# Performance work log

Hardware: AMD Instinct MI355X
Metric: run time of the kernel (lower is better)

Reference implementation:

```python
import jax, jax.numpy as jnp
import numpy as np

B, T, F, H = 128, 1024, 64, 256


def _lstm_cell(x, h, c, W_ih, W_hh, b):
    # x: [B,F], h,c: [B,H]; gate order i,f,g,o (PyTorch convention)
    gates = x @ W_ih.T + h @ W_hh.T + b  # [B,4H]
    i, f, g, o = jnp.split(gates, 4, axis=-1)
    i, f, o = jax.nn.sigmoid(i), jax.nn.sigmoid(f), jax.nn.sigmoid(o)
    g = jnp.tanh(g)
    c = f * c + i * g
    h = o * jnp.tanh(c)
    return h, c


def setup_inputs() -> dict:
    key = jax.random.key(0)
    ks = jax.random.split(key, 10)
    s = 1.0 / np.sqrt(H)
    inp = {
        "ts_batch": jax.random.normal(ks[0], (B, T, F), jnp.float32),
        "W_ih_enc": jax.random.uniform(ks[1], (4 * H, F), jnp.float32, -s, s),
        "W_hh_enc": jax.random.uniform(ks[2], (4 * H, H), jnp.float32, -s, s),
        "b_enc": jax.random.uniform(ks[3], (4 * H,), jnp.float32, -s, s),
        "W_ih_dec": jax.random.uniform(ks[4], (4 * H, F), jnp.float32, -s, s),
        "W_hh_dec": jax.random.uniform(ks[5], (4 * H, H), jnp.float32, -s, s),
        "b_dec": jax.random.uniform(ks[6], (4 * H,), jnp.float32, -s, s),
        "W_out": jax.random.uniform(ks[7], (F, H), jnp.float32, -s, s),
        "b_out": jax.random.uniform(ks[8], (F,), jnp.float32, -s, s),
    }
    return inp


def reference(ts_batch, W_ih_enc, W_hh_enc, b_enc, W_ih_dec, W_hh_dec, b_dec, W_out, b_out):
    batch = ts_batch.shape[0]
    hidden = W_hh_enc.shape[1]
    xs = jnp.swapaxes(ts_batch, 0, 1)  # [T,B,F]

    # ---- encoder: full-sequence LSTM, keep only final (h,c) ----
    def enc_step(carry, x):
        h, c = carry
        h, c = _lstm_cell(x, h, c, W_ih_enc, W_hh_enc, b_enc)
        return (h, c), None

    h0 = jnp.zeros((batch, hidden), ts_batch.dtype)
    (h, c), _ = jax.lax.scan(enc_step, (h0, h0), xs)

    # ---- decoder: iterate timesteps in reverse; emit projection of the
    # hidden state BEFORE consuming the input at that step (training branch) ----
    def dec_step(carry, x):
        h, c = carry
        out = h @ W_out.T + b_out  # [B,F]
        h, c = _lstm_cell(x, h, c, W_ih_dec, W_hh_dec, b_dec)
        return (h, c), out

    _, outs_rev = jax.lax.scan(dec_step, (h, c), xs[::-1])  # [T,B,F], reversed time
    return jnp.swapaxes(outs_rev[::-1], 0, 1)  # [B,T,F]
```

## Files before the change

### kernel.cpp

```cpp
#include <hip/hip_runtime.h>
#include <hip/hip_bf16.h>


#define Bb 128
#define Tt 1024
#define Ff 64
#define Hh 256

typedef _Float16 h16;
typedef __attribute__((ext_vector_type(8))) _Float16 h16x8;
typedef __attribute__((ext_vector_type(4))) float f32x4;

#define WENC_OFF 0
#define WDEC_OFF 327680
#define WOUT_OFF 655360
#define HBUF_OFF 671744
#define FLAGS_BYTE_OFF 1474560

__device__ __forceinline__ float fast_sigmoid(float x) {
  float e = __expf(-fabsf(x));
  float s = __builtin_amdgcn_rcpf(1.f + e);
  return x >= 0.f ? s : 1.f - s;
}
__device__ __forceinline__ float fast_tanh(float x) {
  float e = __expf(-2.f * fabsf(x));
  float r = (1.f - e) * __builtin_amdgcn_rcpf(1.f + e);
  return x >= 0.f ? r : -r;
}

__global__ void lstm_prep(const float* __restrict__ Wih_e, const float* __restrict__ Whh_e,
                          const float* __restrict__ Wih_d, const float* __restrict__ Whh_d,
                          const float* __restrict__ Wout, h16* __restrict__ ws16,
                          unsigned int* __restrict__ flags) {
  int e = blockIdx.x * 256 + threadIdx.x;
  if (e < 16) flags[e] = 0u;
  if (e < 655360) {
    int r = e;
    const float* Wih = Wih_e; const float* Whh = Whh_e;
    int off = WENC_OFF;
    if (r >= 327680) { r -= 327680; Wih = Wih_d; Whh = Whh_d; off = WDEC_OFF; }
    int j    = r & 7;
    int lane = (r >> 3) & 63;
    int kt   = (r >> 9) % 10;
    int tmp  = (r >> 9) / 10;
    int nt   = tmp & 7;
    int w    = (tmp >> 3) & 3;
    int q    = tmp >> 5;
    int g = nt >> 1, ct = nt & 1;
    int col = q * 128 + w * 32 + ct * 16 + (lane & 15);
    int row = g * 256 + col;
    int k = kt * 32 + (lane >> 4) * 8 + j;
    float v = (k < 64) ? Wih[row * 64 + k] : Whh[row * 256 + (k - 64)];
    ws16[off + r] = (h16)v;
  } else if (e < 655360 + 16384) {
    int r = e - 655360;
    int j    = r & 7;
    int lane = (r >> 3) & 63;
    int kt   = (r >> 9) & 7;
    int wt   = (r >> 12) & 1;
    int q    = (r >> 13) & 1;
    int f = q * 32 + wt * 16 + (lane & 15);
    int k = kt * 32 + (lane >> 4) * 8 + j;
    ws16[WOUT_OFF + r] = (h16)Wout[f * 256 + k];
  }
}

__global__ __launch_bounds__(256, 1) void lstm_main(
    const float* __restrict__ ts,
    const float* __restrict__ b_enc, const float* __restrict__ b_dec,
    const float* __restrict__ b_out,
    const h16* __restrict__ wsW, h16* __restrict__ hbuf,
    unsigned int* flags, float* __restrict__ out) {
  const int tid = threadIdx.x;
  const int wg = blockIdx.x;
  const int grp = wg & 7, q = wg >> 3;
  const int w = tid >> 6, lane = tid & 63;
  const int n16 = lane & 15, quad = lane >> 4;
  const int b0 = grp * 16;
  const int partner = wg ^ 8;

  __shared__ h16 xh[2][16][328];
  __shared__ h16x8 woutLds[1024];

  h16x8 wf[8][10];
  {
    const h16x8* wsrc = (const h16x8*)(wsW + WENC_OFF);
#pragma unroll
    for (int nt = 0; nt < 8; ++nt)
#pragma unroll
      for (int kt = 0; kt < 10; ++kt)
        wf[nt][kt] = wsrc[(((q * 4 + w) * 8 + nt) * 10 + kt) * 64 + lane];
  }
  float bias8[8];
#pragma unroll
  for (int nt = 0; nt < 8; ++nt) {
    int g = nt >> 1, ct = nt & 1;
    bias8[nt] = b_enc[g * 256 + q * 128 + w * 32 + ct * 16 + n16];
  }
  const float bo = b_out[q * 32 + w * 16 + n16];

  float c8[8];
#pragma unroll
  for (int i = 0; i < 8; ++i) c8[i] = 0.f;

  for (int i = tid; i < 16 * 264; i += 256) {
    int m = i / 264;
    xh[0][m][64 + (i - m * 264)] = (h16)0.f;
  }
  const int m_x = tid >> 4, ks_x = (tid & 15) * 4;
  {
    const f32x4 xv0 = *(const f32x4*)(ts + ((size_t)(b0 + m_x) * Tt + 0) * Ff + ks_x);
#pragma unroll
    for (int u = 0; u < 4; ++u) xh[0][m_x][ks_x + u] = (h16)xv0[u];
  }
  __syncthreads();

  for (int t = 0; t < 2048; ++t) {
    const int nb = t & 1, nxt = nb ^ 1;
    const bool dec = (t >= 1024);

    if (t > 0) {
      while (__hip_atomic_load(&flags[partner], __ATOMIC_ACQUIRE,
                               __HIP_MEMORY_SCOPE_AGENT) < (unsigned int)t)
        __builtin_amdgcn_s_sleep(1);
    }

    if (t == 1024) {
      const h16x8* wsrc2 = (const h16x8*)(wsW + WDEC_OFF);
#pragma unroll
      for (int nt = 0; nt < 8; ++nt)
#pragma unroll
        for (int kt = 0; kt < 10; ++kt)
          wf[nt][kt] = wsrc2[(((q * 4 + w) * 8 + nt) * 10 + kt) * 64 + lane];
#pragma unroll
      for (int nt = 0; nt < 8; ++nt) {
        int g = nt >> 1, ct = nt & 1;
        bias8[nt] = b_dec[g * 256 + q * 128 + w * 32 + ct * 16 + n16];
      }
      const h16x8* wo = (const h16x8*)(wsW + WOUT_OFF) + q * 1024;
      for (int i = tid; i < 1024; i += 256) woutLds[i] = wo[i];
      __syncthreads();
    }

    h16x8 a[10];
    const h16* xrow = &xh[nb][n16][0];
#pragma unroll
    for (int kt = 0; kt < 2; ++kt)
      a[kt] = *(const h16x8*)(xrow + kt * 32 + quad * 8);
    if (q == 0) {
#pragma unroll
      for (int i = 0; i < 4; ++i)
        a[2 + i] = *(const h16x8*)(xrow + (2 + i) * 32 + quad * 8);
    } else {
#pragma unroll
      for (int i = 0; i < 4; ++i)
        a[6 + i] = *(const h16x8*)(xrow + (6 + i) * 32 + quad * 8);
    }
    if (t > 0) {
      const h16x8* ps = (const h16x8*)(hbuf + ((size_t)partner * 2 + ((t + 1) & 1)) * 2048);
      if (q == 0) {
#pragma unroll
        for (int i = 0; i < 4; ++i) a[6 + i] = ps[n16 * 16 + i * 4 + quad];
      } else {
#pragma unroll
        for (int i = 0; i < 4; ++i) a[2 + i] = ps[n16 * 16 + i * 4 + quad];
      }
    } else {
      h16x8 z;
#pragma unroll
      for (int i = 0; i < 8; ++i) z[i] = (h16)0.f;
      if (q == 0) { a[6] = z; a[7] = z; a[8] = z; a[9] = z; }
      else        { a[2] = z; a[3] = z; a[4] = z; a[5] = z; }
    }

    f32x4 xv;
#pragma unroll
    for (int u = 0; u < 4; ++u) xv[u] = 0.f;
    if (t + 1 < 2048) {
      int xi = (t + 1 < 1024) ? (t + 1) : (2047 - (t + 1));
      xv = *(const f32x4*)(ts + ((size_t)(b0 + m_x) * Tt + xi) * Ff + ks_x);
    }

    f32x4 acc[8];
#pragma unroll
    for (int nt = 0; nt < 8; ++nt) {
      f32x4 v; v[0] = bias8[nt]; v[1] = bias8[nt]; v[2] = bias8[nt]; v[3] = bias8[nt];
      acc[nt] = v;
    }
#pragma unroll
    for (int kt = 0; kt < 10; ++kt)
#pragma unroll
      for (int nt = 0; nt < 8; ++nt)
        acc[nt] = __builtin_amdgcn_mfma_f32_16x16x32_f16(a[kt], wf[nt][kt], acc[nt], 0, 0, 0);

    h16 hv[8];
#pragma unroll
    for (int ct = 0; ct < 2; ++ct)
#pragma unroll
      for (int r = 0; r < 4; ++r) {
        float i_ = fast_sigmoid(acc[0 + ct][r]);
        float f_ = fast_sigmoid(acc[2 + ct][r]);
        float g_ = fast_tanh(acc[4 + ct][r]);
        float o_ = fast_sigmoid(acc[6 + ct][r]);
        float cv = f_ * c8[ct * 4 + r] + i_ * g_;
        c8[ct * 4 + r] = cv;
        hv[ct * 4 + r] = (h16)(o_ * fast_tanh(cv));
      }

    if (dec && w < 2) {
      f32x4 ao; ao[0] = bo; ao[1] = bo; ao[2] = bo; ao[3] = bo;
#pragma unroll
      for (int kt = 0; kt < 8; ++kt)
        ao = __builtin_amdgcn_mfma_f32_16x16x32_f16(a[2 + kt], woutLds[(w * 8 + kt) * 64 + lane], ao, 0, 0, 0);
      int tpos = 2047 - t;
      int f = q * 32 + w * 16 + n16;
#pragma unroll
      for (int r = 0; r < 4; ++r) {
        int m = quad * 4 + r;
        out[((size_t)(b0 + m) * Tt + tpos) * Ff + f] = ao[r];
      }
    }

    {
      h16* hb = hbuf + ((size_t)wg * 2 + (t & 1)) * 2048;
#pragma unroll
      for (int ct = 0; ct < 2; ++ct)
#pragma unroll
        for (int r = 0; r < 4; ++r) {
          int m = quad * 4 + r;
          int colLocal = w * 32 + ct * 16 + n16;
          xh[nxt][m][64 + q * 128 + colLocal] = hv[ct * 4 + r];
          hb[m * 128 + colLocal] = hv[ct * 4 + r];
        }
      if (t + 1 < 2048) {
#pragma unroll
        for (int u = 0; u < 4; ++u) xh[nxt][m_x][ks_x + u] = (h16)xv[u];
      }
    }

    __threadfence();
    __syncthreads();
    if (t < 2047 && tid == 0)
      __hip_atomic_store(&flags[wg], (unsigned int)(t + 1), __ATOMIC_RELEASE,
                         __HIP_MEMORY_SCOPE_AGENT);
  }
}

extern "C" void kernel_launch(void* const* d_in, const int* in_sizes, int n_in,
                              void* d_out, int out_size, void* d_ws, size_t ws_size,
                              hipStream_t stream) {
  const float* ts  = (const float*)d_in[0];
  const float* Wie = (const float*)d_in[1];
  const float* Whe = (const float*)d_in[2];
  const float* be  = (const float*)d_in[3];
  const float* Wid = (const float*)d_in[4];
  const float* Whd = (const float*)d_in[5];
  const float* bd  = (const float*)d_in[6];
  const float* Wo  = (const float*)d_in[7];
  const float* bo  = (const float*)d_in[8];

  h16* ws16 = (h16*)d_ws;
  unsigned int* flags = (unsigned int*)((char*)d_ws + FLAGS_BYTE_OFF);
  float* out = (float*)d_out;

  lstm_prep<<<2624, 256, 0, stream>>>(Wie, Whe, Wid, Whd, Wo, ws16, flags);
  lstm_main<<<16, 256, 0, stream>>>(ts, be, bd, bo, ws16, ws16 + HBUF_OFF, flags, out);
}
```

Baseline: 10.60 ms.

## Overlap local MFMA with partner wait and use per-wave relaxed flag counters

Each workgroup now runs the MFMAs for its own x and h slice before spinning on the partner's flag. The partner's half of h is then loaded with relaxed atomic loads and its MFMAs are finished afterwards. The wait on the partner moves later in the step and the partner-independent work overlaps it. Publishing changes from a threadfence plus single release store to coalesced 64-bit relaxed atomic stores staged through LDS, followed by s_waitcnt and a per-wave fetch_add on padded flag slots. The decoder output projection moves after the publish, off the critical path. The risk is memory-ordering correctness, because relaxed atomics and an empty asm barrier replace the acquire/release semantics.

```diff
diff --git a/kernel.cpp b/kernel.cpp
--- a/kernel.cpp
+++ b/kernel.cpp
@@ -10,6 +10,7 @@
 typedef _Float16 h16;
 typedef __attribute__((ext_vector_type(8))) _Float16 h16x8;
 typedef __attribute__((ext_vector_type(4))) float f32x4;
+typedef unsigned long long u64;
 
 #define WENC_OFF 0
 #define WDEC_OFF 327680
@@ -27,13 +28,18 @@
   float r = (1.f - e) * __builtin_amdgcn_rcpf(1.f + e);
   return x >= 0.f ? r : -r;
 }
+__device__ __forceinline__ h16x8 pack16(u64 lo, u64 hi) {
+  union { u64 u[2]; h16x8 v; } x;
+  x.u[0] = lo; x.u[1] = hi;
+  return x.v;
+}
 
 __global__ void lstm_prep(const float* __restrict__ Wih_e, const float* __restrict__ Whh_e,
                           const float* __restrict__ Wih_d, const float* __restrict__ Whh_d,
                           const float* __restrict__ Wout, h16* __restrict__ ws16,
                           unsigned int* __restrict__ flags) {
   int e = blockIdx.x * 256 + threadIdx.x;
-  if (e < 16) flags[e] = 0u;
+  if (e < 256) flags[e] = 0u;
   if (e < 655360) {
     int r = e;
     const float* Wih = Wih_e; const float* Whh = Whh_e;
@@ -65,6 +71,17 @@
   }
 }
 
+#define MFMA_KT(kt) do {                                                         \
+    acc[0] = __builtin_amdgcn_mfma_f32_16x16x32_f16(a[kt], wf[0][kt], acc[0], 0, 0, 0); \
+    acc[1] = __builtin_amdgcn_mfma_f32_16x16x32_f16(a[kt], wf[1][kt], acc[1], 0, 0, 0); \
+    acc[2] = __builtin_amdgcn_mfma_f32_16x16x32_f16(a[kt], wf[2][kt], acc[2], 0, 0, 0); \
+    acc[3] = __builtin_amdgcn_mfma_f32_16x16x32_f16(a[kt], wf[3][kt], acc[3], 0, 0, 0); \
+    acc[4] = __builtin_amdgcn_mfma_f32_16x16x32_f16(a[kt], wf[4][kt], acc[4], 0, 0, 0); \
+    acc[5] = __builtin_amdgcn_mfma_f32_16x16x32_f16(a[kt], wf[5][kt], acc[5], 0, 0, 0); \
+    acc[6] = __builtin_amdgcn_mfma_f32_16x16x32_f16(a[kt], wf[6][kt], acc[6], 0, 0, 0); \
+    acc[7] = __builtin_amdgcn_mfma_f32_16x16x32_f16(a[kt], wf[7][kt], acc[7], 0, 0, 0); \
+  } while (0)
+
 __global__ __launch_bounds__(256, 1) void lstm_main(
     const float* __restrict__ ts,
     const float* __restrict__ b_enc, const float* __restrict__ b_dec,
@@ -79,7 +96,7 @@
   const int b0 = grp * 16;
   const int partner = wg ^ 8;
 
-  __shared__ h16 xh[2][16][328];
+  __shared__ __align__(16) h16 xh[2][16][328];
   __shared__ h16x8 woutLds[1024];
 
   h16x8 wf[8][10];
@@ -119,12 +136,6 @@
     const int nb = t & 1, nxt = nb ^ 1;
     const bool dec = (t >= 1024);
 
-    if (t > 0) {
-      while (__hip_atomic_load(&flags[partner], __ATOMIC_ACQUIRE,
-                               __HIP_MEMORY_SCOPE_AGENT) < (unsigned int)t)
-        __builtin_amdgcn_s_sleep(1);
-    }
-
     if (t == 1024) {
       const h16x8* wsrc2 = (const h16x8*)(wsW + WDEC_OFF);
 #pragma unroll
@@ -144,34 +155,29 @@
 
     h16x8 a[10];
     const h16* xrow = &xh[nb][n16][0];
-#pragma unroll
-    for (int kt = 0; kt < 2; ++kt)
-      a[kt] = *(const h16x8*)(xrow + kt * 32 + quad * 8);
+    a[0] = *(const h16x8*)(xrow + 0 * 32 + quad * 8);
+    a[1] = *(const h16x8*)(xrow + 1 * 32 + quad * 8);
     if (q == 0) {
-#pragma unroll
-      for (int i = 0; i < 4; ++i)
-        a[2 + i] = *(const h16x8*)(xrow + (2 + i) * 32 + quad * 8);
+      a[2] = *(const h16x8*)(xrow + 2 * 32 + quad * 8);
+      a[3] = *(const h16x8*)(xrow + 3 * 32 + quad * 8);
+      a[4] = *(const h16x8*)(xrow + 4 * 32 + quad * 8);
+      a[5] = *(const h16x8*)(xrow + 5 * 32 + quad * 8);
     } else {
-#pragma unroll
-      for (int i = 0; i < 4; ++i)
-        a[6 + i] = *(const h16x8*)(xrow + (6 + i) * 32 + quad * 8);
-    }
-    if (t > 0) {
-      const h16x8* ps = (const h16x8*)(hbuf + ((size_t)partner * 2 + ((t + 1) & 1)) * 2048);
-      if (q == 0) {
-#pragma unroll
-        for (int i = 0; i < 4; ++i) a[6 + i] = ps[n16 * 16 + i * 4 + quad];
-      } else {
-#pragma unroll
-        for (int i = 0; i < 4; ++i) a[2 + i] = ps[n16 * 16 + i * 4 + quad];
-      }
-    } else {
-      h16x8 z;
-#pragma unroll
-      for (int i = 0; i < 8; ++i) z[i] = (h16)0.f;
-      if (q == 0) { a[6] = z; a[7] = z; a[8] = z; a[9] = z; }
-      else        { a[2] = z; a[3] = z; a[4] = z; a[5] = z; }
-    }
+      a[6] = *(const h16x8*)(xrow + 6 * 32 + quad * 8);
+      a[7] = *(const h16x8*)(xrow + 7 * 32 + quad * 8);
+      a[8] = *(const h16x8*)(xrow + 8 * 32 + quad * 8);
+      a[9] = *(const h16x8*)(xrow + 9 * 32 + quad * 8);
+    }
+
+    f32x4 acc[8];
+#pragma unroll
+    for (int nt = 0; nt < 8; ++nt) {
+      f32x4 v; v[0] = bias8[nt]; v[1] = bias8[nt]; v[2] = bias8[nt]; v[3] = bias8[nt];
+      acc[nt] = v;
+    }
+    MFMA_KT(0); MFMA_KT(1);
+    if (q == 0) { MFMA_KT(2); MFMA_KT(3); MFMA_KT(4); MFMA_KT(5); }
+    else        { MFMA_KT(6); MFMA_KT(7); MFMA_KT(8); MFMA_KT(9); }
 
     f32x4 xv;
 #pragma unroll
@@ -181,17 +187,31 @@
       xv = *(const f32x4*)(ts + ((size_t)(b0 + m_x) * Tt + xi) * Ff + ks_x);
     }
 
-    f32x4 acc[8];
-#pragma unroll
-    for (int nt = 0; nt < 8; ++nt) {
-      f32x4 v; v[0] = bias8[nt]; v[1] = bias8[nt]; v[2] = bias8[nt]; v[3] = bias8[nt];
-      acc[nt] = v;
-    }
-#pragma unroll
-    for (int kt = 0; kt < 10; ++kt)
-#pragma unroll
-      for (int nt = 0; nt < 8; ++nt)
-        acc[nt] = __builtin_amdgcn_mfma_f32_16x16x32_f16(a[kt], wf[nt][kt], acc[nt], 0, 0, 0);
+    if (t > 0) {
+      const unsigned int need = 4u * (unsigned int)t;
+      while (__hip_atomic_load(&flags[partner * 16], __ATOMIC_RELAXED,
+                               __HIP_MEMORY_SCOPE_AGENT) < need) { }
+      asm volatile("" ::: "memory");
+      const u64* ps64 = (const u64*)hbuf + ((size_t)partner * 2 + nxt) * 512;
+      const int jb = (n16 * 16 + quad) * 2;
+      u64 dl0 = __hip_atomic_load((u64*)(ps64 + jb + 0),  __ATOMIC_RELAXED, __HIP_MEMORY_SCOPE_AGENT);
+      u64 dh0 = __hip_atomic_load((u64*)(ps64 + jb + 1),  __ATOMIC_RELAXED, __HIP_MEMORY_SCOPE_AGENT);
+      u64 dl1 = __hip_atomic_load((u64*)(ps64 + jb + 8),  __ATOMIC_RELAXED, __HIP_MEMORY_SCOPE_AGENT);
+      u64 dh1 = __hip_atomic_load((u64*)(ps64 + jb + 9),  __ATOMIC_RELAXED, __HIP_MEMORY_SCOPE_AGENT);
+      u64 dl2 = __hip_atomic_load((u64*)(ps64 + jb + 16), __ATOMIC_RELAXED, __HIP_MEMORY_SCOPE_AGENT);
+      u64 dh2 = __hip_atomic_load((u64*)(ps64 + jb + 17), __ATOMIC_RELAXED, __HIP_MEMORY_SCOPE_AGENT);
+      u64 dl3 = __hip_atomic_load((u64*)(ps64 + jb + 24), __ATOMIC_RELAXED, __HIP_MEMORY_SCOPE_AGENT);
+      u64 dh3 = __hip_atomic_load((u64*)(ps64 + jb + 25), __ATOMIC_RELAXED, __HIP_MEMORY_SCOPE_AGENT);
+      if (q == 0) {
+        a[6] = pack16(dl0, dh0); a[7] = pack16(dl1, dh1);
+        a[8] = pack16(dl2, dh2); a[9] = pack16(dl3, dh3);
+        MFMA_KT(6); MFMA_KT(7); MFMA_KT(8); MFMA_KT(9);
+      } else {
+        a[2] = pack16(dl0, dh0); a[3] = pack16(dl1, dh1);
+        a[4] = pack16(dl2, dh2); a[5] = pack16(dl3, dh3);
+        MFMA_KT(2); MFMA_KT(3); MFMA_KT(4); MFMA_KT(5);
+      }
+    }
 
     h16 hv[8];
 #pragma unroll
@@ -207,6 +227,36 @@
         hv[ct * 4 + r] = (h16)(o_ * fast_tanh(cv));
       }
 
+#pragma unroll
+    for (int ct = 0; ct < 2; ++ct)
+#pragma unroll
+      for (int r = 0; r < 4; ++r) {
+        int m = quad * 4 + r;
+        int colLocal = w * 32 + ct * 16 + n16;
+        xh[nxt][m][64 + q * 128 + colLocal] = hv[ct * 4 + r];
+      }
+    if (t + 1 < 2048) {
+#pragma unroll
+      for (int u = 0; u < 4; ++u) xh[nxt][m_x][ks_x + u] = (h16)xv[u];
+    }
+
+    __syncthreads();
+
+    if (t < 2047) {
+      u64* hb64 = (u64*)hbuf + ((size_t)wg * 2 + nb) * 512;
+#pragma unroll
+      for (int r2 = 0; r2 < 2; ++r2) {
+        const int k = tid + r2 * 256;
+        const int mm = k >> 5, c4 = k & 31;
+        u64 v = *(const u64*)(&xh[nxt][mm][64 + q * 128 + c4 * 4]);
+        __hip_atomic_store(hb64 + k, v, __ATOMIC_RELAXED, __HIP_MEMORY_SCOPE_AGENT);
+      }
+      asm volatile("s_waitcnt vmcnt(0)" ::: "memory");
+      if (lane == 0)
+        __hip_atomic_fetch_add(&flags[wg * 16], 1u, __ATOMIC_RELAXED,
+                               __HIP_MEMORY_SCOPE_AGENT);
+    }
+
     if (dec && w < 2) {
       f32x4 ao; ao[0] = bo; ao[1] = bo; ao[2] = bo; ao[3] = bo;
 #pragma unroll
@@ -220,29 +270,6 @@
         out[((size_t)(b0 + m) * Tt + tpos) * Ff + f] = ao[r];
       }
     }
-
-    {
-      h16* hb = hbuf + ((size_t)wg * 2 + (t & 1)) * 2048;
-#pragma unroll
-      for (int ct = 0; ct < 2; ++ct)
-#pragma unroll
-        for (int r = 0; r < 4; ++r) {
-          int m = quad * 4 + r;
-          int colLocal = w * 32 + ct * 16 + n16;
-          xh[nxt][m][64 + q * 128 + colLocal] = hv[ct * 4 + r];
-          hb[m * 128 + colLocal] = hv[ct * 4 + r];
-        }
-      if (t + 1 < 2048) {
-#pragma unroll
-        for (int u = 0; u < 4; ++u) xh[nxt][m_x][ks_x + u] = (h16)xv[u];
-      }
-    }
-
-    __threadfence();
-    __syncthreads();
-    if (t < 2047 && tid == 0)
-      __hip_atomic_store(&flags[wg], (unsigned int)(t + 1), __ATOMIC_RELEASE,
-                         __HIP_MEMORY_SCOPE_AGENT);
   }
 }
 
```

New measurement: 9.076 ms. 1.17x faster.
